# Performance work log

Measured on AMD Instinct MI355X. Metric: run time of the kernel, lower is better.

The kernel has to match this reference:

```python
import jax, jax.numpy as jnp
import numpy as np

N = 100000
E = 1600000
H = 128       # hidden_channels
HEADS = 8
HD = H // HEADS  # head_dim = 16


def setup_inputs() -> dict:
    key = jax.random.key(0)
    ks = jax.random.split(key, 10)
    x = jax.random.normal(ks[0], (N, H), dtype=jnp.float32)
    gap_edge_index = jax.random.randint(ks[1], (2, E), 0, N, dtype=jnp.int64)
    s = 1.0 / np.sqrt(H)
    Wq = jax.random.normal(ks[2], (H, H), dtype=jnp.float32) * s
    bq = jnp.zeros((H,), dtype=jnp.float32)
    Wk = jax.random.normal(ks[3], (H, H), dtype=jnp.float32) * s
    bk = jnp.zeros((H,), dtype=jnp.float32)
    Wv = jax.random.normal(ks[4], (H, H), dtype=jnp.float32) * s
    bv = jnp.zeros((H,), dtype=jnp.float32)
    Wo = jax.random.normal(ks[5], (H, H), dtype=jnp.float32) * s
    bo = jnp.zeros((H,), dtype=jnp.float32)
    return {"x": x, "gap_edge_index": gap_edge_index,
            "Wq": Wq, "bq": bq, "Wk": Wk, "bk": bk,
            "Wv": Wv, "bv": bv, "Wo": Wo, "bo": bo}


def reference(x, gap_edge_index, Wq, bq, Wk, bk, Wv, bv, Wo, bo):
    n = x.shape[0]
    q = (x @ Wq + bq).reshape(n, HEADS, HD)
    k = (x @ Wk + bk).reshape(n, HEADS, HD)
    v = (x @ Wv + bv).reshape(n, HEADS, HD)
    src, dst = gap_edge_index[0], gap_edge_index[1]
    # per-edge, per-head scores: [E, heads]
    scores = jnp.einsum('ehd,ehd->eh', q[dst], k[src]) / jnp.sqrt(jnp.float32(HD))
    # NOTE: original softmaxes over ALL edges (dim=0), not per-dst segment
    w = jax.nn.softmax(scores, axis=0)
    # scatter-add weighted v[src] into dst: [N, heads, head_dim]
    attended = jax.ops.segment_sum(w[:, :, None] * v[src], dst, num_segments=n)
    attended = attended.reshape(n, HEADS * HD)
    return x + attended @ Wo + bo
```

## Files before the change

kernel.cpp:

```cpp
#include <hip/hip_runtime.h>
#include <cstdint>
#include <cstddef>

#define N_NODES 100000
#define E_EDGES 1600000
#define HCH 128
#define NHEADS 8
#define HDIM 16

typedef unsigned int uint;
typedef unsigned short ushort;
typedef __attribute__((ext_vector_type(8))) short short8;
typedef __attribute__((ext_vector_type(4))) float floatx4;
typedef __attribute__((ext_vector_type(2))) float floatx2;

__device__ __forceinline__ ushort f2bf(float f) {
    uint u = __float_as_uint(f);
    u = (u + 0x7fff + ((u >> 16) & 1)) >> 16;
    return (ushort)u;
}
__device__ __forceinline__ float bflo(uint p) { return __uint_as_float(p << 16); }
__device__ __forceinline__ float bfhi(uint p) { return __uint_as_float(p & 0xffff0000u); }

#define LDSPAD 8
#define SMEM_BYTES (17408 + 34816)

__global__ __launch_bounds__(256) void gemm_qkv(
    const float* __restrict__ A,
    const float* __restrict__ Wq, const float* __restrict__ Wk, const float* __restrict__ Wv,
    const float* __restrict__ bq, const float* __restrict__ bk, const float* __restrict__ bv,
    unsigned char* __restrict__ qe, unsigned char* __restrict__ kvb,
    int M)
{
    __shared__ __align__(16) char smem[SMEM_BYTES];
    ushort (*As)[HCH + LDSPAD] = (ushort(*)[HCH + LDSPAD])smem;
    ushort (*Wt)[HCH + LDSPAD] = (ushort(*)[HCH + LDSPAD])(smem + 17408);
    float (*Cs)[132] = (float(*)[132])(smem + 17408);

    const int t = threadIdx.x;
    const int mb = blockIdx.x * 64;
    const int mode = blockIdx.y;
    const float* W;
    const float* bias;
    if (mode == 0)      { W = Wq; bias = bq; }
    else if (mode == 1) { W = Wk; bias = bk; }
    else                { W = Wv; bias = bv; }

#pragma unroll
    for (int i = 0; i < 8; i++) {
        int p = t + i * 256;
        int row = p >> 5, c4 = p & 31;
        int g = mb + row;
        float4 a4 = make_float4(0.f, 0.f, 0.f, 0.f);
        if (g < M) a4 = *(const float4*)(A + (size_t)g * HCH + c4 * 4);
        uint lo = (uint)f2bf(a4.x) | ((uint)f2bf(a4.y) << 16);
        uint hi = (uint)f2bf(a4.z) | ((uint)f2bf(a4.w) << 16);
        *(uint2*)(&As[row][c4 * 4]) = make_uint2(lo, hi);
    }
#pragma unroll
    for (int i = 0; i < 16; i++) {
        int p = t + i * 256;
        int n = p & 127, k4 = p >> 7;
        float w0 = W[(size_t)(k4 * 4 + 0) * HCH + n];
        float w1 = W[(size_t)(k4 * 4 + 1) * HCH + n];
        float w2 = W[(size_t)(k4 * 4 + 2) * HCH + n];
        float w3 = W[(size_t)(k4 * 4 + 3) * HCH + n];
        uint lo = (uint)f2bf(w0) | ((uint)f2bf(w1) << 16);
        uint hi = (uint)f2bf(w2) | ((uint)f2bf(w3) << 16);
        *(uint2*)(&Wt[n][k4 * 4]) = make_uint2(lo, hi);
    }
    __syncthreads();

    const int lane = t & 63;
    const int w = t >> 6;
    const int m_l = lane & 15;
    const int q_l = lane >> 4;

    floatx4 acc[8];
#pragma unroll
    for (int tl = 0; tl < 8; tl++) acc[tl] = (floatx4){0.f, 0.f, 0.f, 0.f};

#pragma unroll
    for (int ks = 0; ks < HCH; ks += 32) {
        short8 af = *(const short8*)(&As[w * 16 + m_l][ks + q_l * 8]);
#pragma unroll
        for (int tl = 0; tl < 8; tl++) {
            short8 bf = *(const short8*)(&Wt[tl * 16 + m_l][ks + q_l * 8]);
            acc[tl] = __builtin_amdgcn_mfma_f32_16x16x32_bf16(af, bf, acc[tl], 0, 0, 0);
        }
    }
    __syncthreads();

#pragma unroll
    for (int tl = 0; tl < 8; tl++)
#pragma unroll
        for (int r = 0; r < 4; r++)
            Cs[w * 16 + q_l * 4 + r][tl * 16 + m_l] = acc[tl][r];
    __syncthreads();

#pragma unroll
    for (int i = 0; i < 8; i++) {
        int p = t + i * 256;
        int row = p >> 5, c4 = p & 31;
        int g = mb + row;
        if (g >= M) continue;
        float4 b4 = *(const float4*)(bias + c4 * 4);
        float v0 = Cs[row][c4 * 4 + 0] + b4.x;
        float v1 = Cs[row][c4 * 4 + 1] + b4.y;
        float v2 = Cs[row][c4 * 4 + 2] + b4.z;
        float v3 = Cs[row][c4 * 4 + 3] + b4.w;
        int r = __builtin_amdgcn_cvt_pk_fp8_f32(v0, v1, 0, false);
        r = __builtin_amdgcn_cvt_pk_fp8_f32(v2, v3, r, true);
        if (mode == 0) {
            *(int*)(qe + (size_t)g * 128 + c4 * 4) = r;
        } else {
            size_t boff = (size_t)g * 256 + (c4 >> 2) * 32 + ((c4 >> 1) & 1) * 16
                 + (c4 & 1) * 4 + (mode == 2 ? 8 : 0);
            *(int*)(kvb + boff) = r;
        }
    }
}

__global__ __launch_bounds__(256) void gemm_out(
    const ushort* __restrict__ A, const float* __restrict__ W,
    const float* __restrict__ bias, const float* __restrict__ res,
    const float* __restrict__ head_invl,
    float* __restrict__ C, int M)
{
    __shared__ __align__(16) char smem[SMEM_BYTES];
    ushort (*As)[HCH + LDSPAD] = (ushort(*)[HCH + LDSPAD])smem;
    ushort (*Wt)[HCH + LDSPAD] = (ushort(*)[HCH + LDSPAD])(smem + 17408);
    float (*Cs)[132] = (float(*)[132])(smem + 17408);

    const int t = threadIdx.x;
    const int mb = blockIdx.x * 64;

    __shared__ float invl_s[8];
    if (t < 8) invl_s[t] = head_invl[t];
    __syncthreads();

#pragma unroll
    for (int i = 0; i < 8; i++) {
        int p = t + i * 256;
        int row = p >> 5, cu2 = p & 31;
        int g = mb + row;
        uint2 a = make_uint2(0, 0);
        if (g < M) a = *(const uint2*)(A + (size_t)g * HCH + cu2 * 4);
        float invl = invl_s[cu2 >> 2];
        float f0 = bflo(a.x) * invl, f1 = bfhi(a.x) * invl;
        float f2 = bflo(a.y) * invl, f3 = bfhi(a.y) * invl;
        uint lo = (uint)f2bf(f0) | ((uint)f2bf(f1) << 16);
        uint hi = (uint)f2bf(f2) | ((uint)f2bf(f3) << 16);
        *(uint2*)(&As[row][cu2 * 4]) = make_uint2(lo, hi);
    }
#pragma unroll
    for (int i = 0; i < 16; i++) {
        int p = t + i * 256;
        int n = p & 127, k4 = p >> 7;
        float w0 = W[(size_t)(k4 * 4 + 0) * HCH + n];
        float w1 = W[(size_t)(k4 * 4 + 1) * HCH + n];
        float w2 = W[(size_t)(k4 * 4 + 2) * HCH + n];
        float w3 = W[(size_t)(k4 * 4 + 3) * HCH + n];
        uint lo = (uint)f2bf(w0) | ((uint)f2bf(w1) << 16);
        uint hi = (uint)f2bf(w2) | ((uint)f2bf(w3) << 16);
        *(uint2*)(&Wt[n][k4 * 4]) = make_uint2(lo, hi);
    }
    __syncthreads();

    const int lane = t & 63;
    const int w = t >> 6;
    const int m_l = lane & 15;
    const int q_l = lane >> 4;

    floatx4 acc[8];
#pragma unroll
    for (int tl = 0; tl < 8; tl++) acc[tl] = (floatx4){0.f, 0.f, 0.f, 0.f};

#pragma unroll
    for (int ks = 0; ks < HCH; ks += 32) {
        short8 af = *(const short8*)(&As[w * 16 + m_l][ks + q_l * 8]);
#pragma unroll
        for (int tl = 0; tl < 8; tl++) {
            short8 bf = *(const short8*)(&Wt[tl * 16 + m_l][ks + q_l * 8]);
            acc[tl] = __builtin_amdgcn_mfma_f32_16x16x32_bf16(af, bf, acc[tl], 0, 0, 0);
        }
    }
    __syncthreads();

#pragma unroll
    for (int tl = 0; tl < 8; tl++)
#pragma unroll
        for (int r = 0; r < 4; r++)
            Cs[w * 16 + q_l * 4 + r][tl * 16 + m_l] = acc[tl][r];
    __syncthreads();

#pragma unroll
    for (int i = 0; i < 8; i++) {
        int p = t + i * 256;
        int row = p >> 5, c4 = p & 31;
        int g = mb + row;
        if (g >= M) continue;
        float4 b4 = *(const float4*)(bias + c4 * 4);
        float4 r4 = *(const float4*)(res + (size_t)g * HCH + c4 * 4);
        float4 o;
        o.x = Cs[row][c4 * 4 + 0] + b4.x + r4.x;
        o.y = Cs[row][c4 * 4 + 1] + b4.y + r4.y;
        o.z = Cs[row][c4 * 4 + 2] + b4.z + r4.z;
        o.w = Cs[row][c4 * 4 + 3] + b4.w + r4.w;
        *(float4*)(C + (size_t)g * HCH + c4 * 4) = o;
    }
}

constexpr int BSHIFT = 8;
constexpr int NBUCK  = ((N_NODES - 1) >> BSHIFT) + 1;
constexpr int S1_GRID = 256;
constexpr int S1_CH   = (E_EDGES + S1_GRID - 1) / S1_GRID;
constexpr int S2_CAP  = 6144;

__global__ __launch_bounds__(256) void bucket_hist(
    const int* __restrict__ dst, int* __restrict__ bucket_total)
{
    __shared__ int cnt[NBUCK];
    const int t = threadIdx.x;
    for (int b = t; b < NBUCK; b += 256) cnt[b] = 0;
    __syncthreads();
    const int e0 = blockIdx.x * S1_CH;
    const int n = min(S1_CH, E_EDGES - e0);
    for (int i = t; i < n; i += 256)
        atomicAdd(&cnt[dst[e0 + i] >> BSHIFT], 1);
    __syncthreads();
    for (int b = t; b < NBUCK; b += 256)
        if (cnt[b]) atomicAdd(&bucket_total[b], cnt[b]);
}

__global__ __launch_bounds__(512) void bucket_scan(
    const int* __restrict__ bucket_total, int* __restrict__ bucket_start,
    int* __restrict__ bucket_cursor, int* __restrict__ offsets)
{
    __shared__ int s[512];
    const int t = threadIdx.x;
    int v = (t < NBUCK) ? bucket_total[t] : 0;
    s[t] = v;
    __syncthreads();
    for (int off = 1; off < 512; off <<= 1) {
        int a = (t >= off) ? s[t - off] : 0;
        __syncthreads();
        s[t] += a;
        __syncthreads();
    }
    int excl = s[t] - v;
    if (t < NBUCK) { bucket_start[t] = excl; bucket_cursor[t] = excl; }
    if (t == 0) { bucket_start[NBUCK] = E_EDGES; offsets[N_NODES] = E_EDGES; }
}

__global__ __launch_bounds__(256) void sort_scatter1(
    const int* __restrict__ src, const int* __restrict__ dst,
    int* __restrict__ bucket_cursor, int2* __restrict__ tmp)
{
    __shared__ int ls[S1_CH];
    __shared__ int ld[S1_CH];
    __shared__ int cnt[NBUCK];
    const int t = threadIdx.x;
    for (int b = t; b < NBUCK; b += 256) cnt[b] = 0;
    __syncthreads();
    const int e0 = blockIdx.x * S1_CH;
    const int n = min(S1_CH, E_EDGES - e0);
    for (int i = t; i < n; i += 256) {
        int d = dst[e0 + i];
        ls[i] = src[e0 + i];
        ld[i] = d;
        atomicAdd(&cnt[d >> BSHIFT], 1);
    }
    __syncthreads();
    for (int b = t; b < NBUCK; b += 256) {
        int c = cnt[b];
        cnt[b] = c ? atomicAdd(&bucket_cursor[b], c) : 0;
    }
    __syncthreads();
    for (int i = t; i < n; i += 256) {
        int d = ld[i];
        int pos = atomicAdd(&cnt[d >> BSHIFT], 1);
        tmp[pos] = make_int2(ls[i], d);
    }
}

__global__ __launch_bounds__(256) void sort_scatter2(
    const int2* __restrict__ tmp, const int* __restrict__ bucket_start,
    int* __restrict__ psrc, int* __restrict__ offsets)
{
    __shared__ int2 le[S2_CAP];
    __shared__ int cnt[256];
    __shared__ int s[256];
    __shared__ int cur[256];
    const int t = threadIdx.x;
    const int b = blockIdx.x;
    const int bstart = bucket_start[b];
    const int n = bucket_start[b + 1] - bstart;
    cnt[t] = 0;
    __syncthreads();
    for (int i = t; i < n; i += 256) {
        int2 e = tmp[bstart + i];
        if (i < S2_CAP) le[i] = e;
        atomicAdd(&cnt[e.y & 255], 1);
    }
    __syncthreads();
    int v = cnt[t];
    s[t] = v;
    __syncthreads();
    for (int off = 1; off < 256; off <<= 1) {
        int a = (t >= off) ? s[t - off] : 0;
        __syncthreads();
        s[t] += a;
        __syncthreads();
    }
    int excl = s[t] - v;
    int node = (b << BSHIFT) + t;
    if (node < N_NODES) offsets[node] = bstart + excl;
    cur[t] = excl;
    __syncthreads();
    for (int i = t; i < n; i += 256) {
        int2 e = (i < S2_CAP) ? le[i] : tmp[bstart + i];
        int pos = bstart + atomicAdd(&cur[e.y & 255], 1);
        psrc[pos] = e.x;
    }
}

constexpr int FU_BLOCKS = 2048;
constexpr int FU_GROUPS = FU_BLOCKS * 16;

__device__ __forceinline__ float edge_w(
    uint4 e, floatx2 q0, floatx2 q1, floatx2 q2, floatx2 q3)
{
    floatx2 dp = q0 * __builtin_amdgcn_cvt_pk_f32_fp8((int)e.x, false);
    dp += q1 * __builtin_amdgcn_cvt_pk_f32_fp8((int)e.x, true);
    dp += q2 * __builtin_amdgcn_cvt_pk_f32_fp8((int)e.y, false);
    dp += q3 * __builtin_amdgcn_cvt_pk_f32_fp8((int)e.y, true);
    float p = dp.x + dp.y;
    p += __shfl_xor(p, 1);
    return __expf(p * 0.25f);
}
__device__ __forceinline__ void edge_acc(
    uint4 e, float wgt, floatx2& a01, floatx2& a23, floatx2& a45, floatx2& a67)
{
    floatx2 wv = {wgt, wgt};
    a01 += wv * __builtin_amdgcn_cvt_pk_f32_fp8((int)e.z, false);
    a23 += wv * __builtin_amdgcn_cvt_pk_f32_fp8((int)e.z, true);
    a45 += wv * __builtin_amdgcn_cvt_pk_f32_fp8((int)e.w, false);
    a67 += wv * __builtin_amdgcn_cvt_pk_f32_fp8((int)e.w, true);
}

__global__ __launch_bounds__(256) void edge_fused(
    const unsigned char* __restrict__ qe, const unsigned char* __restrict__ kv,
    const int* __restrict__ psrc, const int* __restrict__ offsets,
    ushort* __restrict__ attended, float* __restrict__ block_l)
{
    const int t = threadIdx.x;
    const int sub = t & 15;
    const int gg0 = blockIdx.x * 16 + (t >> 4);

    float lsum = 0.f;

    for (int d = gg0; d < N_NODES; d += FU_GROUPS) {
        const int start = offsets[d];
        const int end   = offsets[d + 1];

        uint2 qw = *(const uint2*)(qe + (size_t)d * 128 + sub * 8);
        floatx2 q0 = __builtin_amdgcn_cvt_pk_f32_fp8((int)qw.x, false);
        floatx2 q1 = __builtin_amdgcn_cvt_pk_f32_fp8((int)qw.x, true);
        floatx2 q2 = __builtin_amdgcn_cvt_pk_f32_fp8((int)qw.y, false);
        floatx2 q3 = __builtin_amdgcn_cvt_pk_f32_fp8((int)qw.y, true);

        floatx2 a01 = {0.f, 0.f}, a23 = {0.f, 0.f}, a45 = {0.f, 0.f}, a67 = {0.f, 0.f};

        for (int i = start; i < end; i += 4) {
            int i1 = min(i + 1, end - 1);
            int i2 = min(i + 2, end - 1);
            int i3 = min(i + 3, end - 1);
            int s0 = psrc[i];
            int s1 = psrc[i1];
            int s2 = psrc[i2];
            int s3 = psrc[i3];
            uint4 e0 = *(const uint4*)(kv + (size_t)s0 * 256 + sub * 16);
            uint4 e1 = *(const uint4*)(kv + (size_t)s1 * 256 + sub * 16);
            uint4 e2 = *(const uint4*)(kv + (size_t)s2 * 256 + sub * 16);
            uint4 e3 = *(const uint4*)(kv + (size_t)s3 * 256 + sub * 16);

            float w0 = edge_w(e0, q0, q1, q2, q3);
            float w1 = edge_w(e1, q0, q1, q2, q3);
            float w2 = edge_w(e2, q0, q1, q2, q3);
            float w3 = edge_w(e3, q0, q1, q2, q3);
            if (i + 1 >= end) w1 = 0.f;
            if (i + 2 >= end) w2 = 0.f;
            if (i + 3 >= end) w3 = 0.f;
            lsum += w0 + w1 + w2 + w3;

            edge_acc(e0, w0, a01, a23, a45, a67);
            edge_acc(e1, w1, a01, a23, a45, a67);
            edge_acc(e2, w2, a01, a23, a45, a67);
            edge_acc(e3, w3, a01, a23, a45, a67);
        }

        uint4 o;
        o.x = (uint)f2bf(a01.x) | ((uint)f2bf(a01.y) << 16);
        o.y = (uint)f2bf(a23.x) | ((uint)f2bf(a23.y) << 16);
        o.z = (uint)f2bf(a45.x) | ((uint)f2bf(a45.y) << 16);
        o.w = (uint)f2bf(a67.x) | ((uint)f2bf(a67.y) << 16);
        *(uint4*)(attended + (size_t)d * HCH + sub * 8) = o;
    }

    __shared__ float sl[256];
    sl[t] = lsum;
    __syncthreads();
    if (t < 8) {
        float L = 0.f;
        for (int base = 0; base < 256; base += 16)
            L += sl[base + 2 * t] + sl[base + 2 * t + 1];
        block_l[blockIdx.x * 8 + t] = 0.5f * L;
    }
}

__global__ __launch_bounds__(256) void reduce_l(
    const float* __restrict__ block_l, float* __restrict__ head_invl, int nblk)
{
    const int t = threadIdx.x;
    float l = 0.f;
    for (int i = t; i < nblk * 8; i += 256) l += block_l[i];
    __shared__ float sl[256];
    sl[t] = l;
    __syncthreads();
    if (t < 8) {
        float L = 0.f;
        for (int i = t; i < 256; i += 8) L += sl[i];
        head_invl[t] = 1.0f / L;
    }
}

extern "C" void kernel_launch(void* const* d_in, const int* in_sizes, int n_in,
                              void* d_out, int out_size, void* d_ws, size_t ws_size,
                              hipStream_t stream)
{
    const float* x  = (const float*)d_in[0];
    const int* eidx = (const int*)d_in[1];
    const float* Wq = (const float*)d_in[2];
    const float* bq = (const float*)d_in[3];
    const float* Wk = (const float*)d_in[4];
    const float* bk = (const float*)d_in[5];
    const float* Wv = (const float*)d_in[6];
    const float* bv = (const float*)d_in[7];
    const float* Wo = (const float*)d_in[8];
    const float* bo = (const float*)d_in[9];
    float* out = (float*)d_out;

    char* ws = (char*)d_ws;
    constexpr size_t SZ_Q8  = (size_t)N_NODES * HCH;
    constexpr size_t SZ_KV8 = (size_t)N_NODES * HCH * 2;
    constexpr size_t SZ_ATT = (size_t)N_NODES * HCH * 2;
    constexpr size_t SZ_PS  = (size_t)E_EDGES * sizeof(int);
    constexpr size_t SZ_TMP = (size_t)E_EDGES * sizeof(int2);
    size_t off = 0;
    unsigned char* qe  = (unsigned char*)(ws + off); off += SZ_Q8;
    unsigned char* kvb = (unsigned char*)(ws + off); off += SZ_KV8;
    ushort* attended = (ushort*)(ws + off); off += SZ_ATT;
    int*    psrc     = (int*)(ws + off);    off += SZ_PS;
    int2*   tmp      = (int2*)(ws + off);   off += SZ_TMP;
    int*    offsets  = (int*)(ws + off);    off += ((size_t)N_NODES + 1) * 4 + 8;
    int*    bucket_total  = (int*)(ws + off); off += (NBUCK + 1) * 4;
    int*    bucket_start  = (int*)(ws + off); off += (NBUCK + 1) * 4;
    int*    bucket_cursor = (int*)(ws + off); off += (NBUCK + 1) * 4;
    float*  block_l   = (float*)(ws + off); off += (size_t)FU_BLOCKS * 8 * sizeof(float);
    float*  head_invl = (float*)(ws + off); off += 32;
    const int* src = eidx;
    const int* dst = eidx + E_EDGES;

    dim3 blk(256);
    const int gblocks = (N_NODES + 63) / 64;

    gemm_qkv<<<dim3(gblocks, 3), blk, 0, stream>>>(x, Wq, Wk, Wv, bq, bk, bv, qe, kvb, N_NODES);

    hipMemsetAsync(bucket_total, 0, (NBUCK + 1) * 4, stream);
    bucket_hist<<<S1_GRID, blk, 0, stream>>>(dst, bucket_total);
    bucket_scan<<<1, 512, 0, stream>>>(bucket_total, bucket_start, bucket_cursor, offsets);
    sort_scatter1<<<S1_GRID, blk, 0, stream>>>(src, dst, bucket_cursor, tmp);
    sort_scatter2<<<NBUCK, blk, 0, stream>>>(tmp, bucket_start, psrc, offsets);

    edge_fused<<<FU_BLOCKS, blk, 0, stream>>>(qe, kvb, psrc, offsets, attended, block_l);
    reduce_l<<<1, blk, 0, stream>>>(block_l, head_invl, FU_BLOCKS);

    gemm_out<<<gblocks, blk, 0, stream>>>(attended, Wo, bo, x, head_invl, out, N_NODES);
}
```

Baseline: 333.4 us.

## Pre-convert weights to bf16 once and fuse K/V projection blocks

Adds a small prep kernel that converts and transposes Wq, Wk, Wv, Wo to bf16 once, so the GEMM blocks no longer redo a strided fp32 weight load and conversion into LDS each time. B fragments are now read directly from global/L2 instead of LDS. K and V are computed in the same block, which reads x once for both, and the grid drops from three y-slices to two. The staging buffer switches from fp32 to bf16 to cut LDS size. The trade-offs are an extra bf16 rounding of the accumulators before the bias is added, and global-memory fragment loads inside the MFMA loop.

```diff
diff --git a/kernel.cpp b/kernel.cpp
--- a/kernel.cpp
+++ b/kernel.cpp
@@ -22,29 +22,41 @@
 __device__ __forceinline__ float bflo(uint p) { return __uint_as_float(p << 16); }
 __device__ __forceinline__ float bfhi(uint p) { return __uint_as_float(p & 0xffff0000u); }
 
-#define LDSPAD 8
-#define SMEM_BYTES (17408 + 34816)
+__global__ __launch_bounds__(256) void prep_w(
+    const float* __restrict__ Wq, const float* __restrict__ Wk,
+    const float* __restrict__ Wv, const float* __restrict__ Wo,
+    ushort* __restrict__ wq_bf, ushort* __restrict__ wkv_bf, ushort* __restrict__ wo_bf)
+{
+    const int t = threadIdx.x;
+    int r = blockIdx.x * 16 + (t >> 4);
+    int k0 = (t & 15) * 8;
+    const float* W; ushort* o; int n, orow;
+    if (r < 128)      { W = Wq; o = wq_bf;  n = r;       orow = r; }
+    else if (r < 256) { W = Wk; o = wkv_bf; n = r - 128; orow = r - 128; }
+    else if (r < 384) { W = Wv; o = wkv_bf; n = r - 256; orow = r - 128; }
+    else              { W = Wo; o = wo_bf;  n = r - 384; orow = r - 384; }
+    uint4 u;
+    u.x = (uint)f2bf(W[(size_t)(k0 + 0) * HCH + n]) | ((uint)f2bf(W[(size_t)(k0 + 1) * HCH + n]) << 16);
+    u.y = (uint)f2bf(W[(size_t)(k0 + 2) * HCH + n]) | ((uint)f2bf(W[(size_t)(k0 + 3) * HCH + n]) << 16);
+    u.z = (uint)f2bf(W[(size_t)(k0 + 4) * HCH + n]) | ((uint)f2bf(W[(size_t)(k0 + 5) * HCH + n]) << 16);
+    u.w = (uint)f2bf(W[(size_t)(k0 + 6) * HCH + n]) | ((uint)f2bf(W[(size_t)(k0 + 7) * HCH + n]) << 16);
+    *(uint4*)(o + (size_t)orow * HCH + k0) = u;
+}
 
 __global__ __launch_bounds__(256) void gemm_qkv(
     const float* __restrict__ A,
-    const float* __restrict__ Wq, const float* __restrict__ Wk, const float* __restrict__ Wv,
+    const ushort* __restrict__ wq_bf, const ushort* __restrict__ wkv_bf,
     const float* __restrict__ bq, const float* __restrict__ bk, const float* __restrict__ bv,
     unsigned char* __restrict__ qe, unsigned char* __restrict__ kvb,
     int M)
 {
-    __shared__ __align__(16) char smem[SMEM_BYTES];
-    ushort (*As)[HCH + LDSPAD] = (ushort(*)[HCH + LDSPAD])smem;
-    ushort (*Wt)[HCH + LDSPAD] = (ushort(*)[HCH + LDSPAD])(smem + 17408);
-    float (*Cs)[132] = (float(*)[132])(smem + 17408);
+    __shared__ __align__(16) char smem[64 * 264 * 2];
+    ushort (*As)[136] = (ushort(*)[136])smem;
+    ushort (*Cs)[264] = (ushort(*)[264])smem;
 
     const int t = threadIdx.x;
     const int mb = blockIdx.x * 64;
-    const int mode = blockIdx.y;
-    const float* W;
-    const float* bias;
-    if (mode == 0)      { W = Wq; bias = bq; }
-    else if (mode == 1) { W = Wk; bias = bk; }
-    else                { W = Wv; bias = bv; }
+    const bool kvmode = (blockIdx.y != 0);
 
 #pragma unroll
     for (int i = 0; i < 8; i++) {
@@ -57,18 +69,6 @@
         uint hi = (uint)f2bf(a4.z) | ((uint)f2bf(a4.w) << 16);
         *(uint2*)(&As[row][c4 * 4]) = make_uint2(lo, hi);
     }
-#pragma unroll
-    for (int i = 0; i < 16; i++) {
-        int p = t + i * 256;
-        int n = p & 127, k4 = p >> 7;
-        float w0 = W[(size_t)(k4 * 4 + 0) * HCH + n];
-        float w1 = W[(size_t)(k4 * 4 + 1) * HCH + n];
-        float w2 = W[(size_t)(k4 * 4 + 2) * HCH + n];
-        float w3 = W[(size_t)(k4 * 4 + 3) * HCH + n];
-        uint lo = (uint)f2bf(w0) | ((uint)f2bf(w1) << 16);
-        uint hi = (uint)f2bf(w2) | ((uint)f2bf(w3) << 16);
-        *(uint2*)(&Wt[n][k4 * 4]) = make_uint2(lo, hi);
-    }
     __syncthreads();
 
     const int lane = t & 63;
@@ -76,61 +76,93 @@
     const int m_l = lane & 15;
     const int q_l = lane >> 4;
 
-    floatx4 acc[8];
-#pragma unroll
-    for (int tl = 0; tl < 8; tl++) acc[tl] = (floatx4){0.f, 0.f, 0.f, 0.f};
-
-#pragma unroll
-    for (int ks = 0; ks < HCH; ks += 32) {
-        short8 af = *(const short8*)(&As[w * 16 + m_l][ks + q_l * 8]);
-#pragma unroll
-        for (int tl = 0; tl < 8; tl++) {
-            short8 bf = *(const short8*)(&Wt[tl * 16 + m_l][ks + q_l * 8]);
-            acc[tl] = __builtin_amdgcn_mfma_f32_16x16x32_bf16(af, bf, acc[tl], 0, 0, 0);
+    if (!kvmode) {
+        floatx4 acc[8];
+#pragma unroll
+        for (int tl = 0; tl < 8; tl++) acc[tl] = (floatx4){0.f, 0.f, 0.f, 0.f};
+#pragma unroll
+        for (int ks = 0; ks < 4; ks++) {
+            short8 af = *(const short8*)(&As[w * 16 + m_l][ks * 32 + q_l * 8]);
+            const ushort* wb = wq_bf + (size_t)m_l * HCH + ks * 32 + q_l * 8;
+#pragma unroll
+            for (int tl = 0; tl < 8; tl++) {
+                short8 bf = *(const short8*)(wb + (size_t)tl * 16 * HCH);
+                acc[tl] = __builtin_amdgcn_mfma_f32_16x16x32_bf16(af, bf, acc[tl], 0, 0, 0);
+            }
         }
-    }
-    __syncthreads();
-
-#pragma unroll
-    for (int tl = 0; tl < 8; tl++)
-#pragma unroll
-        for (int r = 0; r < 4; r++)
-            Cs[w * 16 + q_l * 4 + r][tl * 16 + m_l] = acc[tl][r];
-    __syncthreads();
-
-#pragma unroll
-    for (int i = 0; i < 8; i++) {
-        int p = t + i * 256;
-        int row = p >> 5, c4 = p & 31;
-        int g = mb + row;
-        if (g >= M) continue;
-        float4 b4 = *(const float4*)(bias + c4 * 4);
-        float v0 = Cs[row][c4 * 4 + 0] + b4.x;
-        float v1 = Cs[row][c4 * 4 + 1] + b4.y;
-        float v2 = Cs[row][c4 * 4 + 2] + b4.z;
-        float v3 = Cs[row][c4 * 4 + 3] + b4.w;
-        int r = __builtin_amdgcn_cvt_pk_fp8_f32(v0, v1, 0, false);
-        r = __builtin_amdgcn_cvt_pk_fp8_f32(v2, v3, r, true);
-        if (mode == 0) {
-            *(int*)(qe + (size_t)g * 128 + c4 * 4) = r;
-        } else {
-            size_t boff = (size_t)g * 256 + (c4 >> 2) * 32 + ((c4 >> 1) & 1) * 16
-                 + (c4 & 1) * 4 + (mode == 2 ? 8 : 0);
-            *(int*)(kvb + boff) = r;
+        __syncthreads();
+#pragma unroll
+        for (int tl = 0; tl < 8; tl++)
+#pragma unroll
+            for (int r = 0; r < 4; r++)
+                Cs[w * 16 + q_l * 4 + r][tl * 16 + m_l] = f2bf(acc[tl][r]);
+        __syncthreads();
+#pragma unroll
+        for (int i = 0; i < 4; i++) {
+            int p = t + i * 256;
+            int row = p >> 4, u = p & 15;
+            int g = mb + row;
+            if (g >= M) continue;
+            uint4 c = *(const uint4*)(&Cs[row][u * 8]);
+            float4 b0 = *(const float4*)(bq + u * 8);
+            float4 b1 = *(const float4*)(bq + u * 8 + 4);
+            int r0 = __builtin_amdgcn_cvt_pk_fp8_f32(bflo(c.x) + b0.x, bfhi(c.x) + b0.y, 0, false);
+            r0 = __builtin_amdgcn_cvt_pk_fp8_f32(bflo(c.y) + b0.z, bfhi(c.y) + b0.w, r0, true);
+            int r1 = __builtin_amdgcn_cvt_pk_fp8_f32(bflo(c.z) + b1.x, bfhi(c.z) + b1.y, 0, false);
+            r1 = __builtin_amdgcn_cvt_pk_fp8_f32(bflo(c.w) + b1.z, bfhi(c.w) + b1.w, r1, true);
+            *(uint2*)(qe + (size_t)g * 128 + u * 8) = make_uint2((uint)r0, (uint)r1);
         }
+    } else {
+        floatx4 acc[16];
+#pragma unroll
+        for (int tl = 0; tl < 16; tl++) acc[tl] = (floatx4){0.f, 0.f, 0.f, 0.f};
+#pragma unroll
+        for (int ks = 0; ks < 4; ks++) {
+            short8 af = *(const short8*)(&As[w * 16 + m_l][ks * 32 + q_l * 8]);
+            const ushort* wb = wkv_bf + (size_t)m_l * HCH + ks * 32 + q_l * 8;
+#pragma unroll
+            for (int tl = 0; tl < 16; tl++) {
+                short8 bf = *(const short8*)(wb + (size_t)tl * 16 * HCH);
+                acc[tl] = __builtin_amdgcn_mfma_f32_16x16x32_bf16(af, bf, acc[tl], 0, 0, 0);
+            }
+        }
+        __syncthreads();
+#pragma unroll
+        for (int tl = 0; tl < 16; tl++)
+#pragma unroll
+            for (int r = 0; r < 4; r++)
+                Cs[w * 16 + q_l * 4 + r][tl * 16 + m_l] = f2bf(acc[tl][r]);
+        __syncthreads();
+#pragma unroll
+        for (int i = 0; i < 8; i++) {
+            int p = t + i * 256;
+            int row = p >> 5, u = p & 31;
+            int g = mb + row;
+            if (g >= M) continue;
+            int sub = u >> 1, half = u & 1;
+            int col0 = half * 128 + sub * 8;
+            uint4 c = *(const uint4*)(&Cs[row][col0]);
+            const float* bb = half ? bv : bk;
+            float4 b0 = *(const float4*)(bb + sub * 8);
+            float4 b1 = *(const float4*)(bb + sub * 8 + 4);
+            int r0 = __builtin_amdgcn_cvt_pk_fp8_f32(bflo(c.x) + b0.x, bfhi(c.x) + b0.y, 0, false);
+            r0 = __builtin_amdgcn_cvt_pk_fp8_f32(bflo(c.y) + b0.z, bfhi(c.y) + b0.w, r0, true);
+            int r1 = __builtin_amdgcn_cvt_pk_fp8_f32(bflo(c.z) + b1.x, bfhi(c.z) + b1.y, 0, false);
+            r1 = __builtin_amdgcn_cvt_pk_fp8_f32(bflo(c.w) + b1.z, bfhi(c.w) + b1.w, r1, true);
+            *(uint2*)(kvb + (size_t)g * 256 + u * 8) = make_uint2((uint)r0, (uint)r1);
+        }
     }
 }
 
 __global__ __launch_bounds__(256) void gemm_out(
-    const ushort* __restrict__ A, const float* __restrict__ W,
+    const ushort* __restrict__ A, const ushort* __restrict__ wo_bf,
     const float* __restrict__ bias, const float* __restrict__ res,
     const float* __restrict__ head_invl,
     float* __restrict__ C, int M)
 {
-    __shared__ __align__(16) char smem[SMEM_BYTES];
-    ushort (*As)[HCH + LDSPAD] = (ushort(*)[HCH + LDSPAD])smem;
-    ushort (*Wt)[HCH + LDSPAD] = (ushort(*)[HCH + LDSPAD])(smem + 17408);
-    float (*Cs)[132] = (float(*)[132])(smem + 17408);
+    __shared__ __align__(16) char smem[64 * 136 * 2];
+    ushort (*As)[136] = (ushort(*)[136])smem;
+    ushort (*Cs)[136] = (ushort(*)[136])smem;
 
     const int t = threadIdx.x;
     const int mb = blockIdx.x * 64;
@@ -153,18 +185,6 @@
         uint hi = (uint)f2bf(f2) | ((uint)f2bf(f3) << 16);
         *(uint2*)(&As[row][cu2 * 4]) = make_uint2(lo, hi);
     }
-#pragma unroll
-    for (int i = 0; i < 16; i++) {
-        int p = t + i * 256;
-        int n = p & 127, k4 = p >> 7;
-        float w0 = W[(size_t)(k4 * 4 + 0) * HCH + n];
-        float w1 = W[(size_t)(k4 * 4 + 1) * HCH + n];
-        float w2 = W[(size_t)(k4 * 4 + 2) * HCH + n];
-        float w3 = W[(size_t)(k4 * 4 + 3) * HCH + n];
-        uint lo = (uint)f2bf(w0) | ((uint)f2bf(w1) << 16);
-        uint hi = (uint)f2bf(w2) | ((uint)f2bf(w3) << 16);
-        *(uint2*)(&Wt[n][k4 * 4]) = make_uint2(lo, hi);
-    }
     __syncthreads();
 
     const int lane = t & 63;
@@ -175,39 +195,39 @@
     floatx4 acc[8];
 #pragma unroll
     for (int tl = 0; tl < 8; tl++) acc[tl] = (floatx4){0.f, 0.f, 0.f, 0.f};
-
-#pragma unroll
-    for (int ks = 0; ks < HCH; ks += 32) {
-        short8 af = *(const short8*)(&As[w * 16 + m_l][ks + q_l * 8]);
+#pragma unroll
+    for (int ks = 0; ks < 4; ks++) {
+        short8 af = *(const short8*)(&As[w * 16 + m_l][ks * 32 + q_l * 8]);
+        const ushort* wb = wo_bf + (size_t)m_l * HCH + ks * 32 + q_l * 8;
 #pragma unroll
         for (int tl = 0; tl < 8; tl++) {
-            short8 bf = *(const short8*)(&Wt[tl * 16 + m_l][ks + q_l * 8]);
+            short8 bf = *(const short8*)(wb + (size_t)tl * 16 * HCH);
             acc[tl] = __builtin_amdgcn_mfma_f32_16x16x32_bf16(af, bf, acc[tl], 0, 0, 0);
         }
     }
     __syncthreads();
-
 #pragma unroll
     for (int tl = 0; tl < 8; tl++)
 #pragma unroll
         for (int r = 0; r < 4; r++)
-            Cs[w * 16 + q_l * 4 + r][tl * 16 + m_l] = acc[tl][r];
+            Cs[w * 16 + q_l * 4 + r][tl * 16 + m_l] = f2bf(acc[tl][r]);
     __syncthreads();
 
 #pragma unroll
     for (int i = 0; i < 8; i++) {
         int p = t + i * 256;
-        int row = p >> 5, c4 = p & 31;
+        int row = p >> 5, u = p & 31;
         int g = mb + row;
         if (g >= M) continue;
-        float4 b4 = *(const float4*)(bias + c4 * 4);
-        float4 r4 = *(const float4*)(res + (size_t)g * HCH + c4 * 4);
+        uint2 c = *(const uint2*)(&Cs[row][u * 4]);
+        float4 b4 = *(const float4*)(bias + u * 4);
+        float4 r4 = *(const float4*)(res + (size_t)g * HCH + u * 4);
         float4 o;
-        o.x = Cs[row][c4 * 4 + 0] + b4.x + r4.x;
-        o.y = Cs[row][c4 * 4 + 1] + b4.y + r4.y;
-        o.z = Cs[row][c4 * 4 + 2] + b4.z + r4.z;
-        o.w = Cs[row][c4 * 4 + 3] + b4.w + r4.w;
-        *(float4*)(C + (size_t)g * HCH + c4 * 4) = o;
+        o.x = bflo(c.x) + b4.x + r4.x;
+        o.y = bfhi(c.x) + b4.y + r4.y;
+        o.z = bflo(c.y) + b4.z + r4.z;
+        o.w = bfhi(c.y) + b4.w + r4.w;
+        *(float4*)(C + (size_t)g * HCH + u * 4) = o;
     }
 }
 
@@ -469,13 +489,18 @@
     int*    bucket_cursor = (int*)(ws + off); off += (NBUCK + 1) * 4;
     float*  block_l   = (float*)(ws + off); off += (size_t)FU_BLOCKS * 8 * sizeof(float);
     float*  head_invl = (float*)(ws + off); off += 32;
+    ushort* wq_bf  = (ushort*)(ws + off); off += (size_t)128 * HCH * 2;
+    ushort* wkv_bf = (ushort*)(ws + off); off += (size_t)256 * HCH * 2;
+    ushort* wo_bf  = (ushort*)(ws + off); off += (size_t)128 * HCH * 2;
     const int* src = eidx;
     const int* dst = eidx + E_EDGES;
 
     dim3 blk(256);
     const int gblocks = (N_NODES + 63) / 64;
 
-    gemm_qkv<<<dim3(gblocks, 3), blk, 0, stream>>>(x, Wq, Wk, Wv, bq, bk, bv, qe, kvb, N_NODES);
+    prep_w<<<32, blk, 0, stream>>>(Wq, Wk, Wv, Wo, wq_bf, wkv_bf, wo_bf);
+
+    gemm_qkv<<<dim3(gblocks, 2), blk, 0, stream>>>(x, wq_bf, wkv_bf, bq, bk, bv, qe, kvb, N_NODES);
 
     hipMemsetAsync(bucket_total, 0, (NBUCK + 1) * 4, stream);
     bucket_hist<<<S1_GRID, blk, 0, stream>>>(dst, bucket_total);
@@ -486,5 +511,5 @@
     edge_fused<<<FU_BLOCKS, blk, 0, stream>>>(qe, kvb, psrc, offsets, attended, block_l);
     reduce_l<<<1, blk, 0, stream>>>(block_l, head_invl, FU_BLOCKS);
 
-    gemm_out<<<gblocks, blk, 0, stream>>>(attended, Wo, bo, x, head_invl, out, N_NODES);
-}
+    gemm_out<<<gblocks, blk, 0, stream>>>(attended, wo_bf, bo, x, head_invl, out, N_NODES);
+}
```

Result: slower. 411.0 us (+23.3%).
